# Kernel tuning notes

Measured on AMD Instinct MI355X. Metric: run time of the kernel, lower is better.

Reference implementation:

```python
import jax, jax.numpy as jnp
from jax import lax
import numpy as np

DATA_DIM, DATA_NUM, CTX_DIM, PB_DIM, HID_DIM, T = 6, 30, 180, 2, 240, 8192


def setup_inputs() -> dict:
    key = jax.random.key(0)
    ks = jax.random.split(key, 12)
    f = lambda k, s: jax.random.normal(k, s, dtype=jnp.float32)
    return {
        "data": f(ks[0], (DATA_NUM, DATA_DIM, T)),
        "W1d": f(ks[1], (HID_DIM, DATA_DIM)) * 0.1,
        "b1d": f(ks[2], (HID_DIM,)) * 0.1,
        "W1p": f(ks[3], (HID_DIM, PB_DIM)) * 0.1,
        "b1p": f(ks[4], (HID_DIM,)) * 0.1,
        "W1c": f(ks[5], (HID_DIM, CTX_DIM)) * 0.05,
        "b1c": f(ks[6], (HID_DIM,)) * 0.1,
        "W2d": f(ks[7], (DATA_DIM, HID_DIM)) * 0.1,
        "b2d": f(ks[8], (DATA_DIM,)) * 0.1,
        "W2c": f(ks[9], (CTX_DIM, HID_DIM)) * 0.05,
        "b2c": f(ks[10], (CTX_DIM,)) * 0.1,
        "pb": f(ks[11], (DATA_NUM, PB_DIM)) * 0.1,
    }


def reference(data, W1d, b1d, W1p, b1p, W1c, b1c, W2d, b2d, W2c, b2c, pb):
    # Teacher-forcing path (GENERATE=False): each timestep's input is data[:, :, t];
    # only ctx is carried through the recurrence.
    # Precompute the time-varying + pb input projections for all steps: [T, B, H]
    pre = (jnp.einsum('bdt,hd->tbh', data, W1d) + b1d
           + (pb @ W1p.T + b1p)[None, :, :])

    def step(ctx, pre_t):
        h = jax.nn.relu(pre_t + ctx @ W1c.T + b1c)   # [B, H]
        out = h @ W2d.T + b2d                        # [B, data_dim]
        new_ctx = h @ W2c.T + b2c                    # [B, ctx_dim]
        return new_ctx, out

    ctx0 = jnp.zeros((data.shape[0], CTX_DIM), dtype=data.dtype)
    _, outs = lax.scan(step, ctx0, pre)              # outs: [T, B, data_dim]
    return jnp.transpose(outs, (1, 0, 2))            # [B, T, data_dim] (stack dim=1)
```

## Files before the change

### kernel.cpp

```cpp
#include <hip/hip_runtime.h>
#include <hip/hip_bf16.h>
#include <stdint.h>


#define T_STEPS 8192
#define HID     240
#define CTX     180
#define KTOT    256
#define HXBUF   4096
#define A_HALVES (256*256)
#define SCRATCH_BYTES (A_HALVES*2 + 16)

typedef __hip_bfloat16 bf16;
typedef _Float16 f16;
typedef _Float16 half8  __attribute__((ext_vector_type(8)));
typedef _Float16 half4v __attribute__((ext_vector_type(4)));
typedef float    f32x4  __attribute__((ext_vector_type(4)));
typedef float    f32x2  __attribute__((ext_vector_type(2)));

#define MFMA16(A,B,C) __builtin_amdgcn_mfma_f32_16x16x32_f16((A),(B),(C),0,0,0)

__device__ __forceinline__ float ldin(const void* p, long i, bool f32) {
    return f32 ? ((const float*)p)[i] : __bfloat162float(((const bf16*)p)[i]);
}
__device__ __forceinline__ unsigned pkbf(float a, float b) {
    unsigned ua = (unsigned)__builtin_bit_cast(unsigned short, __float2bfloat16(a));
    unsigned ub = (unsigned)__builtin_bit_cast(unsigned short, __float2bfloat16(b));
    return ua | (ub << 16);
}
__device__ __forceinline__ void barrier_lds() {
    asm volatile("s_waitcnt lgkmcnt(0)\n\ts_barrier" ::: "memory");
}

__device__ __forceinline__ void store_out(void* out, bool f32, int quad, long ob, f32x4 v) {
    if (quad == 0) {
        if (!f32) {
            bf16* op = (bf16*)out + ob;
            *(unsigned*)(op)     = pkbf(v.x, v.y);
            *(unsigned*)(op + 2) = pkbf(v.z, v.w);
        } else {
            float* op = (float*)out + ob;
            f32x2 p0 = {v.x, v.y}; *(f32x2*)(op)     = p0;
            f32x2 p1 = {v.z, v.w}; *(f32x2*)(op + 2) = p1;
        }
    } else if (quad == 1) {
        if (!f32) {
            bf16* op = (bf16*)out + ob;
            *(unsigned*)(op + 4) = pkbf(v.x, v.y);
        } else {
            float* op = (float*)out + ob;
            f32x2 p0 = {v.x, v.y}; *(f32x2*)(op + 4) = p0;
        }
    }
}

__global__ __launch_bounds__(64) void detect_dtype(const void* data, int* flag) {
    unsigned int w  = ((const unsigned int*)data)[threadIdx.x];
    unsigned int lo = w & 0xFFFFu;
    unsigned int ex = (lo >> 7) & 0xFFu;
    unsigned long long huge = __ballot(ex >= 0x8Eu);
    unsigned long long zero = __ballot(lo == 0u);
    if (threadIdx.x == 0) *flag = (huge != 0ull || zero == ~0ull) ? 1 : 0;
}

__global__ __launch_bounds__(256) void build_A(
    const void* __restrict__ W1d, const void* __restrict__ b1d,
    const void* __restrict__ W1p, const void* __restrict__ b1p,
    const void* __restrict__ W1c, const void* __restrict__ b1c,
    const void* __restrict__ W2d, const void* __restrict__ b2d,
    const void* __restrict__ W2c, const void* __restrict__ b2c,
    f16* __restrict__ Aa, const int* __restrict__ flagp)
{
    const bool f32 = (*flagp != 0);
    int idx = blockIdx.x*256 + threadIdx.x;
    int r = idx >> 8, k = idx & 255;
    float v = 0.f;
    if (r < HID) {
        if (k < HID) {
            float acc = 0.f;
            for (int c = 0; c < CTX; ++c)
                acc = fmaf(ldin(W1c, r*CTX+c, f32), ldin(W2c, c*HID+k, f32), acc);
            v = acc;
        } else if (k < 246) {
            v = ldin(W1d, r*6 + (k-240), f32);
        } else if (k == 246) {
            float m0 = 0.f;
            for (int c = 0; c < CTX; ++c)
                m0 = fmaf(ldin(W1c, r*CTX+c, f32), ldin(b2c, c, f32), m0);
            v = ldin(b1d, r, f32) + ldin(b1c, r, f32) + ldin(b1p, r, f32) + m0;
        } else if (k <= 248) {
            v = ldin(W1p, r*2 + (k-247), f32);
        }
    } else if (r < 246) {
        int o = r - 240;
        if (k < HID)       v = ldin(W2d, o*HID + k, f32);
        else if (k == 246) v = ldin(b2d, o, f32);
    }
    Aa[idx] = (f16)v;
}

__device__ __forceinline__ int hx_off(int j, int n) {
    return (j >> 5)*512 + ((((j & 31) >> 3))*16 + n)*8 + (j & 7);
}

__global__ __launch_bounds__(512, 2) void rnn_mfma(
    const void* __restrict__ data,
    const void* __restrict__ b1d, const void* __restrict__ W1p,
    const void* __restrict__ b1p, const void* __restrict__ b1c,
    const void* __restrict__ W1d, const void* __restrict__ pb,
    const f16* __restrict__ Aa, const int* __restrict__ flagp,
    void* __restrict__ out)
{
    const bool f32 = (*flagp != 0);
    const int tid  = threadIdx.x;
    const int w    = tid >> 6;
    const int l    = tid & 63;
    const int n16  = l & 15;
    const int quad = l >> 4;
    const int base = blockIdx.x * 16;
    const int bn   = base + n16;
    const bool bvalid = (bn < 30);
    const long obase = (long)bn * T_STEPS * 6;

    __shared__ __align__(16) f16 Hx[2*HXBUF];

    {
        int* hz = (int*)Hx;
        for (int i = tid; i < HXBUF; i += 512) hz[i] = 0;
    }
    __syncthreads();

    if (tid < 32) {
        int bsel = tid >> 4, n = tid & 15;
        int nb = base + n; if (nb > 29) nb = 29;
        f16* buf = Hx + bsel*HXBUF;
        buf[3584 + (32+n)*8 + 6] = (f16)1.0f;
        buf[3584 + (32+n)*8 + 7] = (f16)ldin(pb, nb*2+0, f32);
        buf[3584 + (48+n)*8 + 0] = (f16)ldin(pb, nb*2+1, f32);
    }

    for (int p = tid; p < HID*16; p += 512) {
        int n = p / HID, j = p - n*HID;
        int nb = base + n; if (nb > 29) nb = 29;
        float s = ldin(b1d, j, f32) + ldin(b1c, j, f32) + ldin(b1p, j, f32)
                + ldin(W1p, j*2+0, f32)*ldin(pb, nb*2+0, f32)
                + ldin(W1p, j*2+1, f32)*ldin(pb, nb*2+1, f32);
        for (int d = 0; d < 6; ++d)
            s = fmaf(ldin(W1d, j*6+d, f32), ldin(data, ((long)nb*6+d)*T_STEPS, f32), s);
        Hx[hx_off(j, n)] = (f16)fmaxf(s, 0.f);
    }

    const int pn = tid & 15, pd = tid >> 4;
    int pnb = base + pn; if (pnb > 29) pnb = 29;
    const long prow = ((long)pnb*6 + (pd < 6 ? pd : 0))*T_STEPS;
    const int  doff = 3584 + (32+pn)*8 + pd;

    if (tid < 96)
        Hx[doff] = (f16)ldin(data, prow + 1, f32);

    unsigned u0 = 0, u1 = 0;
    const unsigned esz = f32 ? 4u : 2u;
    unsigned voff = (unsigned)((unsigned long)(prow + 4) * esz);
    const unsigned vmax = (unsigned)((unsigned long)(prow + T_STEPS-1) * esz);
    if (tid < 96) {
        if (!f32) {
            u0 = ((const unsigned short*)data)[prow + 2];
            u1 = ((const unsigned short*)data)[prow + 3];
        } else {
            u0 = __builtin_bit_cast(unsigned, ((const float*)data)[prow + 2]);
            u1 = __builtin_bit_cast(unsigned, ((const float*)data)[prow + 3]);
        }
    }

    const f16* Ab0 = Aa + (size_t)((w*2+0)*16 + n16)*KTOT + quad*8;
    const f16* Ab1 = Aa + (size_t)((w*2+1)*16 + n16)*KTOT + quad*8;
    half8 a00 = *(const half8*)(Ab0 +   0), a01 = *(const half8*)(Ab0 +  32);
    half8 a02 = *(const half8*)(Ab0 +  64), a03 = *(const half8*)(Ab0 +  96);
    half8 a04 = *(const half8*)(Ab0 + 128), a05 = *(const half8*)(Ab0 + 160);
    half8 a06 = *(const half8*)(Ab0 + 192), a07 = *(const half8*)(Ab0 + 224);
    half8 a10 = *(const half8*)(Ab1 +   0), a11 = *(const half8*)(Ab1 +  32);
    half8 a12 = *(const half8*)(Ab1 +  64), a13 = *(const half8*)(Ab1 +  96);
    half8 a14 = *(const half8*)(Ab1 + 128), a15 = *(const half8*)(Ab1 + 160);
    half8 a16 = *(const half8*)(Ab1 + 192), a17 = *(const half8*)(Ab1 + 224);
    asm volatile("s_waitcnt vmcnt(0)" ::: "memory");
    __syncthreads();

    const f16* hxread0 = Hx + l*8;
    f16* hxw = Hx + w*512 + ((quad>>1)*16 + n16)*8 + 4*(quad&1);

    f32x4 pend = {0.f, 0.f, 0.f, 0.f};

    for (int t2 = 0; t2 < T_STEPS; t2 += 2) {
        #pragma unroll
        for (int s = 0; s < 2; ++s) {
            const int t = t2 + s;
            const int cur = s, nxt = s ^ 1;

            const f16* hxc = hxread0 + cur*HXBUF;
            half8 b0 = *(const half8*)(hxc +    0);
            half8 b1 = *(const half8*)(hxc +  512);
            half8 b2 = *(const half8*)(hxc + 1024);
            half8 b3 = *(const half8*)(hxc + 1536);
            half8 b4 = *(const half8*)(hxc + 2048);
            half8 b5 = *(const half8*)(hxc + 2560);
            half8 b6 = *(const half8*)(hxc + 3072);
            half8 b7 = *(const half8*)(hxc + 3584);

            if (w == 7 && bvalid && (s == 1 || t2 > 0))
                store_out(out, f32, quad, obase + (long)(t-1)*6, pend);

            if (tid < 96) {
                unsigned uc = (s == 0) ? u0 : u1;
                float dv = f32 ? __builtin_bit_cast(float, uc)
                               : __builtin_bit_cast(float, uc << 16);
                Hx[nxt*HXBUF + doff] = (f16)dv;
                unsigned un;
                if (!f32) un = *(const unsigned short*)((const char*)data + voff);
                else      un = __builtin_bit_cast(unsigned, *(const float*)((const char*)data + voff));
                unsigned vn = voff + esz;
                voff = (vn > vmax) ? vmax : vn;
                if (s == 0) u0 = un; else u1 = un;
            }

            f32x4 c0 = {0.f,0.f,0.f,0.f}, c1 = {0.f,0.f,0.f,0.f};
            c0 = MFMA16(a00, b0, c0);
            c1 = MFMA16(a11, b1, c1);
            c0 = MFMA16(a01, b1, c0);
            c1 = MFMA16(a12, b2, c1);
            c0 = MFMA16(a02, b2, c0);
            c1 = MFMA16(a13, b3, c1);
            c0 = MFMA16(a03, b3, c0);
            c1 = MFMA16(a14, b4, c1);
            c0 = MFMA16(a04, b4, c0);
            c1 = MFMA16(a15, b5, c1);
            c0 = MFMA16(a05, b5, c0);
            c1 = MFMA16(a16, b6, c1);
            c0 = MFMA16(a06, b6, c0);
            c1 = MFMA16(a17, b7, c1);
            c0 = MFMA16(a07, b7, c0);

            f16* hxn = hxw + nxt*HXBUF;
            {
                half4v hv;
                hv.x = (f16)fmaxf(c0.x, 0.f);
                hv.y = (f16)fmaxf(c0.y, 0.f);
                hv.z = (f16)fmaxf(c0.z, 0.f);
                hv.w = (f16)fmaxf(c0.w, 0.f);
                *(half4v*)(hxn) = hv;
            }
            c1 = MFMA16(a10, b0, c1);

            if (w < 7) {
                half4v hv;
                hv.x = (f16)fmaxf(c1.x, 0.f);
                hv.y = (f16)fmaxf(c1.y, 0.f);
                hv.z = (f16)fmaxf(c1.z, 0.f);
                hv.w = (f16)fmaxf(c1.w, 0.f);
                *(half4v*)(hxn + 256) = hv;
            } else {
                pend = c1;
            }
            barrier_lds();
        }
    }

    if (w == 7 && bvalid)
        store_out(out, f32, quad, obase + (long)(T_STEPS-1)*6, pend);
}

extern "C" void kernel_launch(void* const* d_in, const int* in_sizes, int n_in,
                              void* d_out, int out_size, void* d_ws, size_t ws_size,
                              hipStream_t stream) {
    const void* data = d_in[0];
    const void* W1d  = d_in[1];
    const void* b1d  = d_in[2];
    const void* W1p  = d_in[3];
    const void* b1p  = d_in[4];
    const void* W1c  = d_in[5];
    const void* b1c  = d_in[6];
    const void* W2d  = d_in[7];
    const void* b2d  = d_in[8];
    const void* W2c  = d_in[9];
    const void* b2c  = d_in[10];
    const void* pb   = d_in[11];

    size_t need = SCRATCH_BYTES;
    char* scratch;
    if (ws_size >= need) {
        scratch = (char*)d_ws;
    } else {
        size_t out_bytes = (size_t)30*T_STEPS*6*sizeof(bf16);
        scratch = (char*)d_out + ((out_bytes - need) & ~(size_t)255);
    }
    f16* Aa    = (f16*)scratch;
    int* flagp = (int*)(scratch + A_HALVES*2);

    detect_dtype<<<1, 64, 0, stream>>>(data, flagp);
    build_A<<<A_HALVES/256, 256, 0, stream>>>(W1d, b1d, W1p, b1p, W1c, b1c,
                                              W2d, b2d, W2c, b2c, Aa, flagp);
    rnn_mfma<<<2, 512, 0, stream>>>(data, b1d, W1p, b1p, b1c, W1d, pb,
                                    Aa, flagp, d_out);
}
```

Measured before the change: 3.654 ms.

## Rotate per-wave MFMA order and prefetch own hidden slice before barrier

Each wave now walks the K-chunks of the recurrent matmul starting at its own slice, and reads the slice it just wrote from LDS before the step barrier, so one B operand is already in registers when the next step starts. The per-wave rotation also spreads the LDS reads of the other chunks across waves, which should reduce bank contention. Both target the latency of the serial per-step LDS-read, MFMA and barrier chain. The cost is a switch on the wave index with eight template instantiations, giving larger code and more register pressure.

```diff
diff --git a/kernel.cpp b/kernel.cpp
--- a/kernel.cpp
+++ b/kernel.cpp
@@ -27,9 +27,6 @@
     unsigned ua = (unsigned)__builtin_bit_cast(unsigned short, __float2bfloat16(a));
     unsigned ub = (unsigned)__builtin_bit_cast(unsigned short, __float2bfloat16(b));
     return ua | (ub << 16);
-}
-__device__ __forceinline__ void barrier_lds() {
-    asm volatile("s_waitcnt lgkmcnt(0)\n\ts_barrier" ::: "memory");
 }
 
 __device__ __forceinline__ void store_out(void* out, bool f32, int quad, long ob, f32x4 v) {
@@ -52,6 +49,32 @@
             f32x2 p0 = {v.x, v.y}; *(f32x2*)(op + 4) = p0;
         }
     }
+}
+
+template<int W0, bool EARLY>
+__device__ __forceinline__ void rot_read(const f16* hxc, half8 b[8], half8 be) {
+    #pragma unroll
+    for (int j = EARLY ? 1 : 0; j < 8; ++j) {
+        const int f = (W0 + j) & 7;
+        b[f] = *(const half8*)(hxc + f*512);
+    }
+    if (EARLY) b[W0] = be;
+}
+
+template<int W0>
+__device__ __forceinline__ void rot_mfma(const half8 A0[8], const half8 A1[8],
+                                         const half8 b[8], f32x4& c0, f32x4& c1,
+                                         half8& lastA, half8& lastB) {
+    #pragma unroll
+    for (int j = 0; j < 8; ++j) {
+        const int f0 = (W0 + j) & 7;
+        c0 = MFMA16(A0[f0], b[f0], c0);
+        if (j < 7) {
+            const int f1 = (W0 + 1 + j) & 7;
+            c1 = MFMA16(A1[f1], b[f1], c1);
+        }
+    }
+    lastA = A1[W0]; lastB = b[W0];
 }
 
 __global__ __launch_bounds__(64) void detect_dtype(const void* data, int* flag) {
@@ -113,7 +136,7 @@
 {
     const bool f32 = (*flagp != 0);
     const int tid  = threadIdx.x;
-    const int w    = tid >> 6;
+    const int w    = __builtin_amdgcn_readfirstlane(tid >> 6);
     const int l    = tid & 63;
     const int n16  = l & 15;
     const int quad = l >> 4;
@@ -174,21 +197,21 @@
 
     const f16* Ab0 = Aa + (size_t)((w*2+0)*16 + n16)*KTOT + quad*8;
     const f16* Ab1 = Aa + (size_t)((w*2+1)*16 + n16)*KTOT + quad*8;
-    half8 a00 = *(const half8*)(Ab0 +   0), a01 = *(const half8*)(Ab0 +  32);
-    half8 a02 = *(const half8*)(Ab0 +  64), a03 = *(const half8*)(Ab0 +  96);
-    half8 a04 = *(const half8*)(Ab0 + 128), a05 = *(const half8*)(Ab0 + 160);
-    half8 a06 = *(const half8*)(Ab0 + 192), a07 = *(const half8*)(Ab0 + 224);
-    half8 a10 = *(const half8*)(Ab1 +   0), a11 = *(const half8*)(Ab1 +  32);
-    half8 a12 = *(const half8*)(Ab1 +  64), a13 = *(const half8*)(Ab1 +  96);
-    half8 a14 = *(const half8*)(Ab1 + 128), a15 = *(const half8*)(Ab1 + 160);
-    half8 a16 = *(const half8*)(Ab1 + 192), a17 = *(const half8*)(Ab1 + 224);
+    half8 A0[8], A1[8];
+    #pragma unroll
+    for (int j = 0; j < 8; ++j) {
+        A0[j] = *(const half8*)(Ab0 + j*32);
+        A1[j] = *(const half8*)(Ab1 + j*32);
+    }
     asm volatile("s_waitcnt vmcnt(0)" ::: "memory");
     __syncthreads();
 
     const f16* hxread0 = Hx + l*8;
+    const f16* hxro    = Hx + w*512 + l*8;
     f16* hxw = Hx + w*512 + ((quad>>1)*16 + n16)*8 + 4*(quad&1);
 
     f32x4 pend = {0.f, 0.f, 0.f, 0.f};
+    half8 b_e = *(const half8*)(hxro);
 
     for (int t2 = 0; t2 < T_STEPS; t2 += 2) {
         #pragma unroll
@@ -197,14 +220,17 @@
             const int cur = s, nxt = s ^ 1;
 
             const f16* hxc = hxread0 + cur*HXBUF;
-            half8 b0 = *(const half8*)(hxc +    0);
-            half8 b1 = *(const half8*)(hxc +  512);
-            half8 b2 = *(const half8*)(hxc + 1024);
-            half8 b3 = *(const half8*)(hxc + 1536);
-            half8 b4 = *(const half8*)(hxc + 2048);
-            half8 b5 = *(const half8*)(hxc + 2560);
-            half8 b6 = *(const half8*)(hxc + 3072);
-            half8 b7 = *(const half8*)(hxc + 3584);
+            half8 b[8];
+            switch (w) {
+                case 0: rot_read<0,true>(hxc, b, b_e); break;
+                case 1: rot_read<1,true>(hxc, b, b_e); break;
+                case 2: rot_read<2,true>(hxc, b, b_e); break;
+                case 3: rot_read<3,true>(hxc, b, b_e); break;
+                case 4: rot_read<4,true>(hxc, b, b_e); break;
+                case 5: rot_read<5,true>(hxc, b, b_e); break;
+                case 6: rot_read<6,true>(hxc, b, b_e); break;
+                default: rot_read<0,false>(hxc, b, b_e); break;
+            }
 
             if (w == 7 && bvalid && (s == 1 || t2 > 0))
                 store_out(out, f32, quad, obase + (long)(t-1)*6, pend);
@@ -223,21 +249,17 @@
             }
 
             f32x4 c0 = {0.f,0.f,0.f,0.f}, c1 = {0.f,0.f,0.f,0.f};
-            c0 = MFMA16(a00, b0, c0);
-            c1 = MFMA16(a11, b1, c1);
-            c0 = MFMA16(a01, b1, c0);
-            c1 = MFMA16(a12, b2, c1);
-            c0 = MFMA16(a02, b2, c0);
-            c1 = MFMA16(a13, b3, c1);
-            c0 = MFMA16(a03, b3, c0);
-            c1 = MFMA16(a14, b4, c1);
-            c0 = MFMA16(a04, b4, c0);
-            c1 = MFMA16(a15, b5, c1);
-            c0 = MFMA16(a05, b5, c0);
-            c1 = MFMA16(a16, b6, c1);
-            c0 = MFMA16(a06, b6, c0);
-            c1 = MFMA16(a17, b7, c1);
-            c0 = MFMA16(a07, b7, c0);
+            half8 lastA, lastB;
+            switch (w) {
+                case 0: rot_mfma<0>(A0, A1, b, c0, c1, lastA, lastB); break;
+                case 1: rot_mfma<1>(A0, A1, b, c0, c1, lastA, lastB); break;
+                case 2: rot_mfma<2>(A0, A1, b, c0, c1, lastA, lastB); break;
+                case 3: rot_mfma<3>(A0, A1, b, c0, c1, lastA, lastB); break;
+                case 4: rot_mfma<4>(A0, A1, b, c0, c1, lastA, lastB); break;
+                case 5: rot_mfma<5>(A0, A1, b, c0, c1, lastA, lastB); break;
+                case 6: rot_mfma<6>(A0, A1, b, c0, c1, lastA, lastB); break;
+                default: rot_mfma<0>(A0, A1, b, c0, c1, lastA, lastB); break;
+            }
 
             f16* hxn = hxw + nxt*HXBUF;
             {
@@ -248,7 +270,7 @@
                 hv.w = (f16)fmaxf(c0.w, 0.f);
                 *(half4v*)(hxn) = hv;
             }
-            c1 = MFMA16(a10, b0, c1);
+            c1 = MFMA16(lastA, lastB, c1);
 
             if (w < 7) {
                 half4v hv;
@@ -260,7 +282,11 @@
             } else {
                 pend = c1;
             }
-            barrier_lds();
+
+            asm volatile("s_waitcnt lgkmcnt(0)" ::: "memory");
+            if (w < 7)
+                b_e = *(const half8*)(hxro + nxt*HXBUF);
+            asm volatile("s_barrier" ::: "memory");
         }
     }
 
```

New measurement: 5.221 ms. +42.9%, slower.
